# Optimization experiments

Measured on AMD Instinct MI355X. Metric: run time of the kernel, lower is better.

The kernel has to match this reference:

```python
import jax, jax.numpy as jnp
from jax import lax
import numpy as np

R = 500          # Resampling: temporal segment width
H = 100          # fixed signal height from the reshape in forward
EPS = 1e-5       # BatchNorm2d default eps
FLAT = 6 * 31 * 32


def _cbrp(x, w, b, g, be, m, v):
    """Conv(5x5, pad 2) + inference BatchNorm + ReLU + MaxPool 2x2."""
    x = lax.conv_general_dilated(x, w, (1, 1), ((2, 2), (2, 2)),
                                 dimension_numbers=('NCHW', 'OIHW', 'NCHW'))
    x = x + b[None, :, None, None]
    inv = g * lax.rsqrt(v + EPS)
    x = x * inv[None, :, None, None] + (be - m * inv)[None, :, None, None]
    x = jax.nn.relu(x)
    return lax.reduce_window(x, -jnp.inf, lax.max, (1, 1, 2, 2), (1, 1, 2, 2), 'VALID')


def setup_inputs() -> dict:
    key = jax.random.key(0)
    ks = jax.random.split(key, 16)
    d = {}
    d['x'] = jax.random.normal(ks[0], (16, 1, 100, 4000), dtype=jnp.float32)
    chans = [(1, 16), (16, 32), (32, 64), (64, 32)]
    for i, (ci, co) in enumerate(chans, start=1):
        fan_in = ci * 25
        d[f'w{i}'] = jax.random.normal(ks[i], (co, ci, 5, 5), dtype=jnp.float32) * np.float32((2.0 / fan_in) ** 0.5)
        d[f'b{i}'] = jnp.zeros((co,), jnp.float32)
        d[f'g{i}'] = jnp.ones((co,), jnp.float32)
        d[f'be{i}'] = jnp.zeros((co,), jnp.float32)
        d[f'm{i}'] = jnp.zeros((co,), jnp.float32)
        d[f'v{i}'] = jnp.ones((co,), jnp.float32)
    d['fw1'] = jax.random.normal(ks[5], (32, FLAT), dtype=jnp.float32) * np.float32(FLAT ** -0.5)
    d['fb1'] = jnp.zeros((32,), jnp.float32)
    d['fw2'] = jax.random.normal(ks[6], (2, 32), dtype=jnp.float32) * np.float32(32 ** -0.5)
    d['fb2'] = jnp.zeros((2,), jnp.float32)
    return d


def reference(x, w1, b1, g1, be1, m1, v1,
              w2, b2, g2, be2, m2, v2,
              w3, b3, g3, be3, m3, v3,
              w4, b4, g4, be4, m4, v4,
              fw1, fb1, fw2, fb2):
    B = x.shape[0]
    L = x.shape[-1] // R  # number of temporal segments per sample
    # (B,1,100,L*R) -> (B*L,1,100,R): batch all segments into one conv call
    xs = x[:, 0].reshape(B, H, L, R).transpose(0, 2, 1, 3).reshape(B * L, 1, H, R)
    h = _cbrp(xs, w1, b1, g1, be1, m1, v1)   # (BL,16,50,250)
    h = _cbrp(h, w2, b2, g2, be2, m2, v2)    # (BL,32,25,125)
    h = _cbrp(h, w3, b3, g3, be3, m3, v3)    # (BL,64,12,62)
    h = _cbrp(h, w4, b4, g4, be4, m4, v4)    # (BL,32,6,31)
    h = h.reshape(B * L, FLAT)
    h = h @ fw1.T + fb1
    h = h @ fw2.T + fb2                      # (BL,2)
    return h.reshape(B, L, 2).mean(axis=1)   # average segment votes per sample
```

## Files before the change

kernel.cpp:

```cpp
#include <hip/hip_runtime.h>
#include <hip/hip_bf16.h>

#define EPSB 1e-5f

typedef short s16x8 __attribute__((ext_vector_type(8)));
typedef float f32x16 __attribute__((ext_vector_type(16)));

#define P1_OFF   0
#define P2_OFF   57507840
#define P3_OFF   89817088
#define L4_OFF   107642880
#define H1_OFF   110690304
#define WT2_OFF  110706688
#define WT3_OFF  110732288
#define WT4_OFF  110834688
#define SS2_OFF  110937088
#define SS3_OFF  110937344
#define SS4_OFF  110937856

__device__ __forceinline__ unsigned short bf16bits(float f) {
    __hip_bfloat16 h = __float2bfloat16(f);
    union { __hip_bfloat16 h; unsigned short u; } cv; cv.h = h; return cv.u;
}


template<int HP, int WP, int C, int IH, int IW>
__device__ __forceinline__ void pad_body(__hip_bfloat16* __restrict__ buf, int idx)
{
    if (idx >= 128 * HP * WP) return;
    const int rc = idx % (HP * WP);
    const int row = rc / WP, col = rc % WP;
    const bool pad = (row < 2) | (row >= 2 + IH) | (col < 2) | (col >= 2 + IW);
    if (!pad) return;
    int4* p = reinterpret_cast<int4*>(buf + (size_t)idx * C);
    #pragma unroll
    for (int i = 0; i < C * 2 / 16; ++i) p[i] = int4{0, 0, 0, 0};
}

__device__ __forceinline__ void wtrans_body(const float* __restrict__ src,
                                            __hip_bfloat16* __restrict__ dst,
                                            int CO, int CI, int idx)
{
    if (idx >= CO * CI * 25) return;
    const int co  = idx / (CI * 25);
    const int rem = idx % (CI * 25);
    const int ci  = rem / 25;
    const int tap = rem % 25;
    dst[((size_t)tap * CO + co) * CI + ci] = __float2bfloat16(src[idx]);
}

__device__ __forceinline__ void scsh_body(const float* __restrict__ b,
                                          const float* __restrict__ g,
                                          const float* __restrict__ be,
                                          const float* __restrict__ m,
                                          const float* __restrict__ v,
                                          float* __restrict__ out, int CO, int i)
{
    if (i < CO) {
        const float sc = g[i] * rsqrtf(v[i] + EPSB);
        out[i]      = sc;
        out[CO + i] = fmaf(b[i] - m[i], sc, be[i]);
    }
}

__global__ __launch_bounds__(256)
void prep_kernel(__hip_bfloat16* p1, __hip_bfloat16* p2, __hip_bfloat16* p3,
                 const float* w2, __hip_bfloat16* wt2,
                 const float* w3, __hip_bfloat16* wt3,
                 const float* w4, __hip_bfloat16* wt4,
                 const float* b2, const float* g2, const float* be2,
                 const float* m2, const float* v2, float* ss2,
                 const float* b3, const float* g3, const float* be3,
                 const float* m3, const float* v3, float* ss3,
                 const float* b4, const float* g4, const float* be4,
                 const float* m4, const float* v4, float* ss4)
{
    const int bid = blockIdx.x;
    const int tid = threadIdx.x;
    if      (bid < 7020) pad_body<54, 260, 16, 50, 250>(p1, bid * 256 + tid);
    else if (bid < 8992) pad_body<29, 136, 32, 25, 125>(p2, (bid - 7020) * 256 + tid);
    else if (bid < 9536) pad_body<16,  68, 64, 12,  62>(p3, (bid - 8992) * 256 + tid);
    else if (bid < 9586) wtrans_body(w2, wt2, 32, 16, (bid - 9536) * 256 + tid);
    else if (bid < 9786) wtrans_body(w3, wt3, 64, 32, (bid - 9586) * 256 + tid);
    else if (bid < 9986) wtrans_body(w4, wt4, 32, 64, (bid - 9786) * 256 + tid);
    else {
        const int which = bid - 9986;
        if      (which == 0) scsh_body(b2, g2, be2, m2, v2, ss2, 32, tid);
        else if (which == 1) scsh_body(b3, g3, be3, m3, v3, ss3, 64, tid);
        else                 scsh_body(b4, g4, be4, m4, v4, ss4, 32, tid);
    }
}

__global__ __launch_bounds__(256, 1)
void conv1_kernel(const float* __restrict__ x,
                  const float* __restrict__ wgt,
                  const float* __restrict__ bias,
                  const float* __restrict__ g,
                  const float* __restrict__ be,
                  const float* __restrict__ m,
                  const float* __restrict__ v,
                  __hip_bfloat16* __restrict__ p1)
{
    const int n   = blockIdx.y;
    const int idx = blockIdx.x * 256 + threadIdx.x;
    if (idx >= 50 * 250) return;
    const int ph = idx / 250, pw = idx % 250;

    const int b = n >> 3, l = n & 7;
    const float* ib = x + (size_t)b * 400000 + l * 500;

    const int h0  = 2 * ph - 2;
    const int w0c = 2 * pw - 2;
    float win[6][6];
    #pragma unroll
    for (int r = 0; r < 6; ++r) {
        const int hh = h0 + r;
        const bool vr = (hh >= 0) & (hh < 100);
        #pragma unroll
        for (int c = 0; c < 6; ++c) {
            const int ww = w0c + c;
            const bool ok = vr & (ww >= 0) & (ww < 500);
            win[r][c] = ok ? ib[hh * 4000 + ww] : 0.0f;
        }
    }
    #pragma unroll
    for (int r = 0; r < 6; ++r)
        #pragma unroll
        for (int c = 0; c < 6; ++c)
            asm volatile("" : "+v"(win[r][c]));

    int packed[8];
    #pragma unroll
    for (int cp = 0; cp < 8; ++cp) {
        unsigned short h2[2];
        #pragma unroll
        for (int sub = 0; sub < 2; ++sub) {
            const int co = 2 * cp + sub;
            float a0 = 0.f, a1 = 0.f, a2 = 0.f, a3 = 0.f;
            #pragma unroll
            for (int kh = 0; kh < 5; ++kh) {
                #pragma unroll
                for (int kw = 0; kw < 5; ++kw) {
                    const float w = wgt[co * 25 + kh * 5 + kw];
                    a0 = fmaf(w, win[kh  ][kw  ], a0);
                    a1 = fmaf(w, win[kh  ][kw+1], a1);
                    a2 = fmaf(w, win[kh+1][kw  ], a2);
                    a3 = fmaf(w, win[kh+1][kw+1], a3);
                }
            }
            const float sc = g[co] * rsqrtf(v[co] + EPSB);
            const float sh = fmaf(bias[co] - m[co], sc, be[co]);
            #define RA(a) fmaxf(fmaf((a), sc, sh), 0.0f)
            h2[sub] = bf16bits(fmaxf(fmaxf(RA(a0), RA(a1)), fmaxf(RA(a2), RA(a3))));
            #undef RA
        }
        packed[cp] = h2[0] | (h2[1] << 16);
    }

    int4* dst = reinterpret_cast<int4*>(
        p1 + (size_t)n * (54 * 260 * 16) + ((2 + ph) * 260 + (2 + pw)) * 16);
    dst[0] = int4{packed[0], packed[1], packed[2], packed[3]};
    dst[1] = int4{packed[4], packed[5], packed[6], packed[7]};
}

template<int CI, int CO, int HINP, int WINP, int HOUTP, int WOUTP,
         int PH, int PW, int NT, int NCOT, int RPW, bool NCHW_OUT>
__global__ __launch_bounds__(256)
void conv_mfma(const __hip_bfloat16* __restrict__ pin,
               const __hip_bfloat16* __restrict__ wq,
               const float* __restrict__ scsh,
               void* __restrict__ pout)
{
    constexpr int R = (PH + RPW - 1) / RPW;
    constexpr int NROW = 2 * RPW + 4;
    const int lane = threadIdx.x & 63;
    int t = blockIdx.x * 4 + (threadIdx.x >> 6);
    const int cot = t % NCOT; t /= NCOT;
    const int wt  = t % NT;   t /= NT;
    const int r   = t % R;    t /= R;
    const int n   = t;
    if (n >= 128) return;

    const int lw = lane & 31, loct = lane >> 5;
    const int co0 = cot * 32;
    const int w0  = wt * 32;

    const __hip_bfloat16* bbase = pin + (size_t)n * (HINP * WINP * CI)
                                + (w0 + lw) * CI + loct * 8;
    const __hip_bfloat16* abase = wq + (co0 + lw) * CI + loct * 8;

    f32x16 acc[2 * RPW];
    #pragma unroll
    for (int q = 0; q < 2 * RPW; ++q) acc[q] = (f32x16){};

    #pragma unroll
    for (int kw = 0; kw < 5; ++kw) {
        #pragma unroll
        for (int s = 0; s < CI / 16; ++s) {
            s16x8 bfr[NROW];
            #pragma unroll
            for (int j = 0; j < NROW; ++j) {
                const int row = (2 * RPW * r + j < HINP) ? (2 * RPW * r + j) : (HINP - 1);
                bfr[j] = *reinterpret_cast<const s16x8*>(bbase + (row * WINP + kw) * CI + s * 16);
            }
            #pragma unroll
            for (int kh = 0; kh < 5; ++kh) {
                const s16x8 a = *reinterpret_cast<const s16x8*>(
                    abase + (size_t)((kh * 5 + kw) * CO) * CI + s * 16);
                #pragma unroll
                for (int q = 0; q < 2 * RPW; ++q)
                    acc[q] = __builtin_amdgcn_mfma_f32_32x32x16_bf16(a, bfr[kh + q], acc[q], 0, 0, 0);
            }
        }
    }

    const int pw = wt * 16 + (lw >> 1);
    const bool act = ((lane & 1) == 0) && (pw < PW);
    #pragma unroll
    for (int p = 0; p < RPW; ++p) {
        const int pr = RPW * r + p;
        const bool rok = (pr < PH);
        #pragma unroll
        for (int reg = 0; reg < 16; ++reg) {
            const int co = co0 + (reg & 3) + 8 * (reg >> 2) + 4 * loct;
            const float sc = scsh[co], sh = scsh[CO + co];
            const float v0 = fmaxf(fmaf(acc[2 * p    ][reg], sc, sh), 0.0f);
            const float v1 = fmaxf(fmaf(acc[2 * p + 1][reg], sc, sh), 0.0f);
            float vm = fmaxf(v0, v1);
            vm = fmaxf(vm, __shfl_xor(vm, 1, 64));
            if (act && rok) {
                if (NCHW_OUT) {
                    ((float*)pout)[(((size_t)n * CO + co) * PH + pr) * PW + pw] = vm;
                } else {
                    ((__hip_bfloat16*)pout)[(size_t)n * (HOUTP * WOUTP * CO)
                        + ((2 + pr) * WOUTP + (2 + pw)) * CO + co] = __float2bfloat16(vm);
                }
            }
        }
    }
}

__global__ __launch_bounds__(64)
void fc1_kernel(const float* __restrict__ h,
                const float* __restrict__ fw1,
                const float* __restrict__ fb1,
                float* __restrict__ h1)
{
    const int n = blockIdx.x;
    const int j = blockIdx.y;
    const int lane = threadIdx.x;
    const float* hp = h   + (size_t)n * 5952;
    const float* wp = fw1 + (size_t)j * 5952;
    float s = 0.0f;
    for (int k = lane; k < 5952; k += 64) s = fmaf(hp[k], wp[k], s);
    #pragma unroll
    for (int off = 32; off > 0; off >>= 1) s += __shfl_down(s, off, 64);
    if (lane == 0) h1[n * 32 + j] = s + fb1[j];
}

__global__ __launch_bounds__(64)
void fc2_mean_kernel(const float* __restrict__ h1,
                     const float* __restrict__ fw2,
                     const float* __restrict__ fb2,
                     float* __restrict__ out)
{
    const int t = threadIdx.x;
    if (t >= 32) return;
    const int b = t >> 1, c = t & 1;
    float s = 0.0f;
    for (int l = 0; l < 8; ++l) {
        const float* hp = h1 + (size_t)(b * 8 + l) * 32;
        #pragma unroll
        for (int j = 0; j < 32; ++j) s = fmaf(hp[j], fw2[c * 32 + j], s);
    }
    out[t] = fmaf(s, 0.125f, fb2[c]);
}

extern "C" void kernel_launch(void* const* d_in, const int* in_sizes, int n_in,
                              void* d_out, int out_size, void* d_ws, size_t ws_size,
                              hipStream_t stream)
{
    const float* x   = (const float*)d_in[0];
    const float* w1  = (const float*)d_in[1];
    const float* b1  = (const float*)d_in[2];
    const float* g1  = (const float*)d_in[3];
    const float* be1 = (const float*)d_in[4];
    const float* m1  = (const float*)d_in[5];
    const float* v1  = (const float*)d_in[6];
    const float* w2  = (const float*)d_in[7];
    const float* b2  = (const float*)d_in[8];
    const float* g2  = (const float*)d_in[9];
    const float* be2 = (const float*)d_in[10];
    const float* m2  = (const float*)d_in[11];
    const float* v2  = (const float*)d_in[12];
    const float* w3  = (const float*)d_in[13];
    const float* b3  = (const float*)d_in[14];
    const float* g3  = (const float*)d_in[15];
    const float* be3 = (const float*)d_in[16];
    const float* m3  = (const float*)d_in[17];
    const float* v3  = (const float*)d_in[18];
    const float* w4  = (const float*)d_in[19];
    const float* b4  = (const float*)d_in[20];
    const float* g4  = (const float*)d_in[21];
    const float* be4 = (const float*)d_in[22];
    const float* m4  = (const float*)d_in[23];
    const float* v4  = (const float*)d_in[24];
    const float* fw1 = (const float*)d_in[25];
    const float* fb1 = (const float*)d_in[26];
    const float* fw2 = (const float*)d_in[27];
    const float* fb2 = (const float*)d_in[28];

    char* ws = (char*)d_ws;
    __hip_bfloat16* p1  = (__hip_bfloat16*)(ws + P1_OFF);
    __hip_bfloat16* p2  = (__hip_bfloat16*)(ws + P2_OFF);
    __hip_bfloat16* p3  = (__hip_bfloat16*)(ws + P3_OFF);
    float*          l4  = (float*)(ws + L4_OFF);
    float*          h1  = (float*)(ws + H1_OFF);
    __hip_bfloat16* wt2 = (__hip_bfloat16*)(ws + WT2_OFF);
    __hip_bfloat16* wt3 = (__hip_bfloat16*)(ws + WT3_OFF);
    __hip_bfloat16* wt4 = (__hip_bfloat16*)(ws + WT4_OFF);
    float*          ss2 = (float*)(ws + SS2_OFF);
    float*          ss3 = (float*)(ws + SS3_OFF);
    float*          ss4 = (float*)(ws + SS4_OFF);

    prep_kernel<<<dim3(9989), 256, 0, stream>>>(
        p1, p2, p3, w2, wt2, w3, wt3, w4, wt4,
        b2, g2, be2, m2, v2, ss2,
        b3, g3, be3, m3, v3, ss3,
        b4, g4, be4, m4, v4, ss4);

    conv1_kernel<<<dim3(49, 128), 256, 0, stream>>>(x, w1, b1, g1, be1, m1, v1, p1);

    conv_mfma<16, 32, 54, 260, 29, 136, 25, 125, 8, 1, 2, false>
        <<<dim3(128 * 13 * 8 / 4), 256, 0, stream>>>(p1, wt2, ss2, p2);
    conv_mfma<32, 64, 29, 136, 16, 68, 12, 62, 4, 2, 2, false>
        <<<dim3(128 * 6 * 4 * 2 / 4), 256, 0, stream>>>(p2, wt3, ss3, p3);
    conv_mfma<64, 32, 16, 68, 0, 0, 6, 31, 2, 1, 1, true>
        <<<dim3(128 * 6 * 2 / 4), 256, 0, stream>>>(p3, wt4, ss4, l4);

    fc1_kernel<<<dim3(128, 32), 64, 0, stream>>>(l4, fw1, fb1, h1);
    fc2_mean_kernel<<<1, 64, 0, stream>>>(h1, fw2, fb2, (float*)d_out);
}
```

Measured before the change: 456.6 us.

## Split conv1 pooling quad across four threads with shuffle max reduction

Conv1 now assigns one thread per pre-pool output pixel instead of one per pooled pixel, launching four times as many threads, and combines the 2x2 max-pool with cross-lane shuffles. Weights are pre-transposed to tap-major layout and BN scale/shift are precomputed in the prep kernel, so conv1 no longer recomputes rsqrt per channel. This raises parallelism and lowers per-thread register pressure (the launch bound that capped occupancy is dropped), but it loses the overlapping-window input reuse, so each thread issues its own 25 loads and the total load count grows.

```diff
diff --git a/kernel.cpp b/kernel.cpp
--- a/kernel.cpp
+++ b/kernel.cpp
@@ -17,6 +17,8 @@
 #define SS2_OFF  110937088
 #define SS3_OFF  110937344
 #define SS4_OFF  110937856
+#define WT1_OFF  110938112
+#define SS1_OFF  110939712
 
 __device__ __forceinline__ unsigned short bf16bits(float f) {
     __hip_bfloat16 h = __float2bfloat16(f);
@@ -61,6 +63,14 @@
         out[i]      = sc;
         out[CO + i] = fmaf(b[i] - m[i], sc, be[i]);
     }
+}
+
+__device__ __forceinline__ void wt1_body(const float* __restrict__ src,
+                                         float* __restrict__ dst, int idx)
+{
+    if (idx >= 400) return;
+    const int tap = idx >> 4, co = idx & 15;
+    dst[idx] = src[co * 25 + tap];
 }
 
 __global__ __launch_bounds__(256)
@@ -73,7 +83,10 @@
                  const float* b3, const float* g3, const float* be3,
                  const float* m3, const float* v3, float* ss3,
                  const float* b4, const float* g4, const float* be4,
-                 const float* m4, const float* v4, float* ss4)
+                 const float* m4, const float* v4, float* ss4,
+                 const float* b1, const float* g1, const float* be1,
+                 const float* m1, const float* v1, float* ss1,
+                 const float* w1, float* wt1)
 {
     const int bid = blockIdx.x;
     const int tid = threadIdx.x;
@@ -83,84 +96,75 @@
     else if (bid < 9586) wtrans_body(w2, wt2, 32, 16, (bid - 9536) * 256 + tid);
     else if (bid < 9786) wtrans_body(w3, wt3, 64, 32, (bid - 9586) * 256 + tid);
     else if (bid < 9986) wtrans_body(w4, wt4, 32, 64, (bid - 9786) * 256 + tid);
-    else {
+    else if (bid < 9990) {
         const int which = bid - 9986;
         if      (which == 0) scsh_body(b2, g2, be2, m2, v2, ss2, 32, tid);
         else if (which == 1) scsh_body(b3, g3, be3, m3, v3, ss3, 64, tid);
-        else                 scsh_body(b4, g4, be4, m4, v4, ss4, 32, tid);
-    }
-}
-
-__global__ __launch_bounds__(256, 1)
+        else if (which == 2) scsh_body(b4, g4, be4, m4, v4, ss4, 32, tid);
+        else                 scsh_body(b1, g1, be1, m1, v1, ss1, 16, tid);
+    } else {
+        wt1_body(w1, wt1, (bid - 9990) * 256 + tid);
+    }
+}
+
+__global__ __launch_bounds__(256)
 void conv1_kernel(const float* __restrict__ x,
-                  const float* __restrict__ wgt,
-                  const float* __restrict__ bias,
-                  const float* __restrict__ g,
-                  const float* __restrict__ be,
-                  const float* __restrict__ m,
-                  const float* __restrict__ v,
+                  const float* __restrict__ wt1,
+                  const float* __restrict__ ss1,
                   __hip_bfloat16* __restrict__ p1)
 {
     const int n   = blockIdx.y;
     const int idx = blockIdx.x * 256 + threadIdx.x;
-    if (idx >= 50 * 250) return;
-    const int ph = idx / 250, pw = idx % 250;
+    const int q     = idx >> 2;
+    const int sub   = idx & 3;
+    const int ph = q / 250, pw = q % 250;
+    const int h = 2 * ph + (sub >> 1);
+    const int w = 2 * pw + (sub & 1);
 
     const int b = n >> 3, l = n & 7;
     const float* ib = x + (size_t)b * 400000 + l * 500;
 
-    const int h0  = 2 * ph - 2;
-    const int w0c = 2 * pw - 2;
-    float win[6][6];
-    #pragma unroll
-    for (int r = 0; r < 6; ++r) {
-        const int hh = h0 + r;
+    float acc[16];
+    #pragma unroll
+    for (int co = 0; co < 16; ++co) acc[co] = 0.0f;
+
+    #pragma unroll
+    for (int kh = 0; kh < 5; ++kh) {
+        const int hh = h - 2 + kh;
         const bool vr = (hh >= 0) & (hh < 100);
         #pragma unroll
-        for (int c = 0; c < 6; ++c) {
-            const int ww = w0c + c;
+        for (int kw = 0; kw < 5; ++kw) {
+            const int ww = w - 2 + kw;
             const bool ok = vr & (ww >= 0) & (ww < 500);
-            win[r][c] = ok ? ib[hh * 4000 + ww] : 0.0f;
+            const float val = ok ? ib[hh * 4000 + ww] : 0.0f;
+            const float* wr = wt1 + (kh * 5 + kw) * 16;
+            #pragma unroll
+            for (int co = 0; co < 16; ++co)
+                acc[co] = fmaf(wr[co], val, acc[co]);
         }
     }
-    #pragma unroll
-    for (int r = 0; r < 6; ++r)
-        #pragma unroll
-        for (int c = 0; c < 6; ++c)
-            asm volatile("" : "+v"(win[r][c]));
 
     int packed[8];
     #pragma unroll
     for (int cp = 0; cp < 8; ++cp) {
-        unsigned short h2[2];
-        #pragma unroll
-        for (int sub = 0; sub < 2; ++sub) {
-            const int co = 2 * cp + sub;
-            float a0 = 0.f, a1 = 0.f, a2 = 0.f, a3 = 0.f;
-            #pragma unroll
-            for (int kh = 0; kh < 5; ++kh) {
-                #pragma unroll
-                for (int kw = 0; kw < 5; ++kw) {
-                    const float w = wgt[co * 25 + kh * 5 + kw];
-                    a0 = fmaf(w, win[kh  ][kw  ], a0);
-                    a1 = fmaf(w, win[kh  ][kw+1], a1);
-                    a2 = fmaf(w, win[kh+1][kw  ], a2);
-                    a3 = fmaf(w, win[kh+1][kw+1], a3);
-                }
-            }
-            const float sc = g[co] * rsqrtf(v[co] + EPSB);
-            const float sh = fmaf(bias[co] - m[co], sc, be[co]);
-            #define RA(a) fmaxf(fmaf((a), sc, sh), 0.0f)
-            h2[sub] = bf16bits(fmaxf(fmaxf(RA(a0), RA(a1)), fmaxf(RA(a2), RA(a3))));
-            #undef RA
+        unsigned short hb[2];
+        #pragma unroll
+        for (int s = 0; s < 2; ++s) {
+            const int co = 2 * cp + s;
+            float vv = fmaxf(fmaf(acc[co], ss1[co], ss1[16 + co]), 0.0f);
+            vv = fmaxf(vv, __shfl_xor(vv, 1, 64));
+            vv = fmaxf(vv, __shfl_xor(vv, 2, 64));
+            hb[s] = bf16bits(vv);
         }
-        packed[cp] = h2[0] | (h2[1] << 16);
-    }
-
-    int4* dst = reinterpret_cast<int4*>(
-        p1 + (size_t)n * (54 * 260 * 16) + ((2 + ph) * 260 + (2 + pw)) * 16);
-    dst[0] = int4{packed[0], packed[1], packed[2], packed[3]};
-    dst[1] = int4{packed[4], packed[5], packed[6], packed[7]};
+        packed[cp] = hb[0] | (hb[1] << 16);
+    }
+
+    if (sub == 0 && q < 12500) {
+        int4* dst = reinterpret_cast<int4*>(
+            p1 + (size_t)n * (54 * 260 * 16) + ((2 + ph) * 260 + (2 + pw)) * 16);
+        dst[0] = int4{packed[0], packed[1], packed[2], packed[3]};
+        dst[1] = int4{packed[4], packed[5], packed[6], packed[7]};
+    }
 }
 
 template<int CI, int CO, int HINP, int WINP, int HOUTP, int WOUTP,
@@ -322,14 +326,18 @@
     float*          ss2 = (float*)(ws + SS2_OFF);
     float*          ss3 = (float*)(ws + SS3_OFF);
     float*          ss4 = (float*)(ws + SS4_OFF);
-
-    prep_kernel<<<dim3(9989), 256, 0, stream>>>(
+    float*          wt1 = (float*)(ws + WT1_OFF);
+    float*          ss1 = (float*)(ws + SS1_OFF);
+
+    prep_kernel<<<dim3(9992), 256, 0, stream>>>(
         p1, p2, p3, w2, wt2, w3, wt3, w4, wt4,
         b2, g2, be2, m2, v2, ss2,
         b3, g3, be3, m3, v3, ss3,
-        b4, g4, be4, m4, v4, ss4);
-
-    conv1_kernel<<<dim3(49, 128), 256, 0, stream>>>(x, w1, b1, g1, be1, m1, v1, p1);
+        b4, g4, be4, m4, v4, ss4,
+        b1, g1, be1, m1, v1, ss1,
+        w1, wt1);
+
+    conv1_kernel<<<dim3(196, 128), 256, 0, stream>>>(x, wt1, ss1, p1);
 
     conv_mfma<16, 32, 54, 260, 29, 136, 25, 125, 8, 1, 2, false>
         <<<dim3(128 * 13 * 8 / 4), 256, 0, stream>>>(p1, wt2, ss2, p2);
```

New measurement: 569.3 us. 24.7% more time.
